# Optimization experiments

Hardware: AMD Instinct MI355X
Metric: run time of the kernel (lower is better)

Reference implementation:

```python
import jax, jax.numpy as jnp
import numpy as np

B, S = 64, 1024
D_INPUT, D_POLAR, N_LAYERS, KAN, N_CLASSES = 256, 256, 8, 32, 1000
PI = float(np.pi)
EPS = 1e-8


def _gelu(v):
    return jax.nn.gelu(v, approximate=False)  # torch nn.GELU default = exact erf


def setup_inputs() -> dict:
    key = jax.random.key(0)
    ks = jax.random.split(key, 16)

    def rn(k, shape, fan_in):
        return jax.random.normal(k, shape, jnp.float32) / np.sqrt(fan_in)

    return {
        "x": jax.random.normal(ks[0], (B, S, D_INPUT), jnp.float32),
        "embed_w": rn(ks[1], (D_INPUT, 2 * D_POLAR), D_INPUT),
        "embed_b": jnp.zeros((2 * D_POLAR,), jnp.float32),
        "mag_w1": rn(ks[2], (N_LAYERS, 1, KAN), 1),
        "mag_b1": jnp.zeros((N_LAYERS, KAN), jnp.float32),
        "mag_w2": rn(ks[3], (N_LAYERS, KAN, 1), KAN),
        "mag_b2": jnp.zeros((N_LAYERS, 1), jnp.float32),
        "ph_w1": rn(ks[4], (N_LAYERS, 2, KAN), 2),
        "ph_b1": jnp.zeros((N_LAYERS, KAN), jnp.float32),
        "ph_w2": rn(ks[5], (N_LAYERS, KAN, 2), KAN),
        "ph_b2": jnp.zeros((N_LAYERS, 2), jnp.float32),
        "cls_w1": rn(ks[6], (D_POLAR, KAN), D_POLAR),
        "cls_b1": jnp.zeros((KAN,), jnp.float32),
        "cls_w2": rn(ks[7], (KAN, N_CLASSES), KAN),
        "cls_b2": jnp.zeros((N_CLASSES,), jnp.float32),
    }


def _forward(x, embed_w, embed_b, mag_w1, mag_b1, mag_w2, mag_b2,
             ph_w1, ph_b1, ph_w2, ph_b2, cls_w1, cls_b1, cls_w2, cls_b2):
    h = x @ embed_w + embed_b                      # [B,S,2D]
    r = jnp.abs(h[..., :D_POLAR]) + 0.1            # [B,S,D]
    theta = h[..., D_POLAR:] * PI                  # [B,S,D]
    for i in range(N_LAYERS):
        xc = r * jnp.cos(theta)
        yc = r * jnp.sin(theta)
        xm = xc.mean(axis=1, keepdims=True)        # [B,1,D]
        ym = yc.mean(axis=1, keepdims=True)
        r_agg = jnp.sqrt(xm * xm + ym * ym + EPS)
        th_agg = jnp.arctan2(ym, xm)
        # magnitude MLP (1 -> 32 -> 1) in log space, per channel
        log_r = jnp.log(r_agg + EPS)[..., None]    # [B,1,D,1]
        lr = _gelu(log_r @ mag_w1[i] + mag_b1[i]) @ mag_w2[i] + mag_b2[i]
        r_trans = jnp.exp(lr[..., 0])              # [B,1,D]
        # phase MLP (2 -> 32 -> 2) on (sin, cos)
        pin = jnp.stack([jnp.sin(th_agg), jnp.cos(th_agg)], axis=-1)  # [B,1,D,2]
        pout = _gelu(pin @ ph_w1[i] + ph_b1[i]) @ ph_w2[i] + ph_b2[i]
        norm = jnp.sqrt(pout[..., 0] ** 2 + pout[..., 1] ** 2 + EPS)
        th_trans = jnp.arctan2(pout[..., 0] / norm, pout[..., 1] / norm)
        x_out = xc + r_trans * jnp.cos(th_trans)
        y_out = yc + r_trans * jnp.sin(th_trans)
        r = jnp.sqrt(x_out * x_out + y_out * y_out + EPS)
        theta = jnp.arctan2(y_out, x_out)
    pooled = r.mean(axis=1)                        # [B,D]
    return _gelu(pooled @ cls_w1 + cls_b1) @ cls_w2 + cls_b2  # [B,n_classes]


def reference(x, embed_w, embed_b, mag_w1, mag_b1, mag_w2, mag_b2,
              ph_w1, ph_b1, ph_w2, ph_b2, cls_w1, cls_b1, cls_w2, cls_b2):
    return _forward(x, embed_w, embed_b, mag_w1, mag_b1, mag_w2, mag_b2,
                    ph_w1, ph_b1, ph_w2, ph_b2, cls_w1, cls_b1, cls_w2, cls_b2)
```

## Files before the change

kernel.cpp:

```cpp
#include <hip/hip_runtime.h>
#include <hip/hip_bf16.h>
#include <hip/hip_fp16.h>

#define EPS 1e-8f
#define PI_F 3.14159265358979323846f

typedef _Float16 half8 __attribute__((ext_vector_type(8)));
typedef _Float16 half4 __attribute__((ext_vector_type(4)));
typedef float f32x4 __attribute__((ext_vector_type(4)));
typedef float f32x2 __attribute__((ext_vector_type(2)));

__device__ __forceinline__ float gelu_exact(float v) {
    return 0.5f * v * (1.0f + erff(v * 0.70710678118654752f));
}

__global__ void convertW(const float* __restrict__ W,
                         _Float16* __restrict__ Wth, _Float16* __restrict__ Wtl,
                         float* __restrict__ zero_base) {
    int idx = blockIdx.x * 256 + threadIdx.x;
    if (idx < 49152) zero_base[idx] = 0.f;
    int col = idx & 511, k = idx >> 9;
    int d = col & 255, g = d >> 6;
    int j = g * 128 + ((col < 256) ? (d & 63) : (64 + (d & 63)));
    float f = W[k * 512 + col];
    _Float16 h = (_Float16)f;
    Wth[j * 256 + k] = h;
    Wtl[j * 256 + k] = (_Float16)(f - (float)h);
}

__global__ __launch_bounds__(256, 4) void gemm_embed(
    const float* __restrict__ x,
    const _Float16* __restrict__ Wth, const _Float16* __restrict__ Wtl,
    const float* __restrict__ bias,
    unsigned short* __restrict__ XY8,
    float* __restrict__ XMsum, float* __restrict__ YMsum)
{
    __shared__ __attribute__((aligned(16))) _Float16 Ah[4096], Al[4096], Bh[4096], Bl[4096];
    const int tid  = threadIdx.x;
    const int wave = tid >> 6;
    const int lane = tid & 63;
    const int id   = blockIdx.x;
    const int xcd  = id & 7;
    const int s    = id >> 3;
    const int g    = s & 3;
    const int mt   = (s >> 2) * 8 + xcd;
    const int m0   = mt * 128;
    const int q    = lane >> 4, ln = lane & 15;

    f32x4 acc[8][2];
#pragma unroll
    for (int mi = 0; mi < 8; ++mi) {
        acc[mi][0] = (f32x4){0.f, 0.f, 0.f, 0.f};
        acc[mi][1] = (f32x4){0.f, 0.f, 0.f, 0.f};
    }

    for (int kt = 0; kt < 8; ++kt) {
        __syncthreads();
#pragma unroll
        for (int c2 = 0; c2 < 2; ++c2) {
            int idx = c2 * 256 + tid;
            int r = idx >> 2, c = idx & 3;
            size_t go = (size_t)(g * 128 + r) * 256 + kt * 32 + c * 8;
            half8 vh = *(const half8*)(Wth + go);
            half8 vl = *(const half8*)(Wtl + go);
            int pos = c ^ ((r >> 1) & 3);
            *(half8*)&Bh[r * 32 + pos * 8] = vh;
            *(half8*)&Bl[r * 32 + pos * 8] = vl;
        }
#pragma unroll
        for (int L = 0; L < 2; ++L) {
            int idx = L * 256 + tid;
            int r = idx >> 2, cq = idx & 3;
            const float* src = x + (size_t)(m0 + r) * 256 + kt * 32 + cq * 8;
            const float4 f0 = *(const float4*)(src);
            const float4 f1 = *(const float4*)(src + 4);
            half8 hh, ll;
            hh[0] = (_Float16)f0.x; ll[0] = (_Float16)(f0.x - (float)hh[0]);
            hh[1] = (_Float16)f0.y; ll[1] = (_Float16)(f0.y - (float)hh[1]);
            hh[2] = (_Float16)f0.z; ll[2] = (_Float16)(f0.z - (float)hh[2]);
            hh[3] = (_Float16)f0.w; ll[3] = (_Float16)(f0.w - (float)hh[3]);
            hh[4] = (_Float16)f1.x; ll[4] = (_Float16)(f1.x - (float)hh[4]);
            hh[5] = (_Float16)f1.y; ll[5] = (_Float16)(f1.y - (float)hh[5]);
            hh[6] = (_Float16)f1.z; ll[6] = (_Float16)(f1.z - (float)hh[6]);
            hh[7] = (_Float16)f1.w; ll[7] = (_Float16)(f1.w - (float)hh[7]);
            int pos = cq ^ ((r >> 1) & 3);
            *(half8*)&Ah[r * 32 + pos * 8] = hh;
            *(half8*)&Al[r * 32 + pos * 8] = ll;
        }
        __syncthreads();

        half8 bh[2], bl[2], am[8];
#pragma unroll
        for (int t = 0; t < 2; ++t) {
            int rn = (t * 4 + wave) * 16 + ln;
            int off = rn * 32 + (q ^ ((rn >> 1) & 3)) * 8;
            bh[t] = *(const half8*)&Bh[off];
            bl[t] = *(const half8*)&Bl[off];
        }
#pragma unroll
        for (int mi = 0; mi < 8; ++mi) {
            int row = mi * 16 + ln;
            am[mi] = *(const half8*)&Ah[row * 32 + (q ^ ((row >> 1) & 3)) * 8];
        }
#pragma unroll
        for (int mi = 0; mi < 8; ++mi)
#pragma unroll
            for (int t = 0; t < 2; ++t)
                acc[mi][t] = __builtin_amdgcn_mfma_f32_16x16x32_f16(am[mi], bh[t], acc[mi][t], 0, 0, 0);
#pragma unroll
        for (int mi = 0; mi < 8; ++mi)
#pragma unroll
            for (int t = 0; t < 2; ++t)
                acc[mi][t] = __builtin_amdgcn_mfma_f32_16x16x32_f16(am[mi], bl[t], acc[mi][t], 0, 0, 0);
#pragma unroll
        for (int mi = 0; mi < 8; ++mi) {
            int row = mi * 16 + ln;
            half8 alv = *(const half8*)&Al[row * 32 + (q ^ ((row >> 1) & 3)) * 8];
#pragma unroll
            for (int t = 0; t < 2; ++t)
                acc[mi][t] = __builtin_amdgcn_mfma_f32_16x16x32_f16(alv, bh[t], acc[mi][t], 0, 0, 0);
        }
    }

    const int d  = g * 64 + wave * 16 + ln;
    const int b  = m0 >> 10;
    const float b1 = bias[d];
    const float b2 = bias[256 + d];
    float sx = 0.f, sy = 0.f;
#pragma unroll
    for (int mi = 0; mi < 8; ++mi) {
#pragma unroll
        for (int i = 0; i < 4; ++i) {
            const int row = m0 + mi * 16 + q * 4 + i;
            const float h1 = acc[mi][0][i] + b1;
            const float h2 = acc[mi][1][i] + b2;
            const float rr = fabsf(h1) + 0.1f;
            float sv, cv;
            __sincosf(PI_F * h2, &sv, &cv);
            const float xc = rr * cv, yc = rr * sv;
            int pk = __builtin_amdgcn_cvt_pk_fp8_f32(xc, yc, 0, false);
            XY8[(size_t)row * 256 + d] = (unsigned short)pk;
            sx += xc; sy += yc;
        }
    }
    sx += __shfl_down(sx, 32); sx += __shfl_down(sx, 16);
    sy += __shfl_down(sy, 32); sy += __shfl_down(sy, 16);
    if (lane < 16) {
        atomicAdd(&XMsum[b * 256 + d], sx);
        atomicAdd(&YMsum[b * 256 + d], sy);
    }
}

__global__ __launch_bounds__(256) void layers_kernel(
    const float* __restrict__ XMsum, const float* __restrict__ YMsum,
    const float* __restrict__ mw1, const float* __restrict__ mb1,
    const float* __restrict__ mw2, const float* __restrict__ mb2,
    const float* __restrict__ pw1, const float* __restrict__ pb1,
    const float* __restrict__ pw2, const float* __restrict__ pb2,
    float* __restrict__ DX, float* __restrict__ DY)
{
    __shared__ float s_mw1[256], s_mb1[256], s_mw2[256], s_mb2[8];
    __shared__ float s_pw1[512], s_pb1[256], s_pw2[512], s_pb2[16];
    const int tid = threadIdx.x;
    s_mw1[tid] = mw1[tid]; s_mb1[tid] = mb1[tid];
    s_mw2[tid] = mw2[tid]; s_pb1[tid] = pb1[tid];
    s_pw1[tid] = pw1[tid]; s_pw1[256 + tid] = pw1[256 + tid];
    s_pw2[tid] = pw2[tid]; s_pw2[256 + tid] = pw2[256 + tid];
    if (tid < 8)  s_mb2[tid] = mb2[tid];
    if (tid < 16) s_pb2[tid] = pb2[tid];
    __syncthreads();

    const int gid = blockIdx.x * 256 + tid;
    const int idx = gid >> 3;
    const int sub = gid & 7;
    float xm = XMsum[idx] * (1.0f / 1024.0f);
    float ym = YMsum[idx] * (1.0f / 1024.0f);
    float dxa = 0.f, dya = 0.f;
#pragma unroll 1
    for (int i = 0; i < 8; ++i) {
        float r2    = xm * xm + ym * ym;
        float r_agg = sqrtf(r2 + EPS);
        float hyp   = sqrtf(r2);
        float inv   = hyp > 0.f ? 1.0f / hyp : 0.f;
        float st    = ym * inv;
        float ct    = hyp > 0.f ? xm * inv : 1.0f;
        float log_r = logf(r_agg + EPS);
        float lr = 0.f, p0 = 0.f, p1 = 0.f;
#pragma unroll
        for (int k4 = 0; k4 < 4; ++k4) {
            int k = sub * 4 + k4;
            float hm = gelu_exact(log_r * s_mw1[i * 32 + k] + s_mb1[i * 32 + k]);
            lr += hm * s_mw2[i * 32 + k];
            float hp = gelu_exact(st * s_pw1[i * 64 + k] + ct * s_pw1[i * 64 + 32 + k] + s_pb1[i * 32 + k]);
            p0 += hp * s_pw2[i * 64 + 2 * k + 0];
            p1 += hp * s_pw2[i * 64 + 2 * k + 1];
        }
        lr += __shfl_xor(lr, 1); lr += __shfl_xor(lr, 2); lr += __shfl_xor(lr, 4);
        p0 += __shfl_xor(p0, 1); p0 += __shfl_xor(p0, 2); p0 += __shfl_xor(p0, 4);
        p1 += __shfl_xor(p1, 1); p1 += __shfl_xor(p1, 2); p1 += __shfl_xor(p1, 4);
        lr += s_mb2[i];
        p0 += s_pb2[i * 2 + 0];
        p1 += s_pb2[i * 2 + 1];
        float r_trans = expf(lr);
        float hp2  = sqrtf(p0 * p0 + p1 * p1);
        float invp = hp2 > 0.f ? 1.0f / hp2 : 0.f;
        float ctt  = hp2 > 0.f ? p1 * invp : 1.0f;
        float stt  = p0 * invp;
        float dx = r_trans * ctt;
        float dy = r_trans * stt;
        dxa += dx; dya += dy; xm += dx; ym += dy;
    }
    if (sub == 0) { DX[idx] = dxa; DY[idx] = dya; }
}

__global__ __launch_bounds__(256) void pool_kernel(
    const unsigned short* __restrict__ XY8,
    const float* __restrict__ DX, const float* __restrict__ DY,
    float* __restrict__ pooled)
{
    __shared__ float red[256][9];
    const int b = blockIdx.x, sc = blockIdx.y, tid = threadIdx.x;
    const int dg = tid & 31;
    const int sh = tid >> 5;
    const int d0 = dg * 8;
    float dxv[8], dyv[8], s[8];
#pragma unroll
    for (int j = 0; j < 8; ++j) {
        dxv[j] = DX[b * 256 + d0 + j];
        dyv[j] = DY[b * 256 + d0 + j];
        s[j] = 0.f;
    }
    const int r0 = sc * 128 + sh * 16;
    const size_t base = ((size_t)b * 1024 + r0) * 256 + d0;
#pragma unroll 4
    for (int i = 0; i < 16; ++i) {
        const int4 v = *(const int4*)(XY8 + base + (size_t)i * 256);
        const int wv[4] = {v.x, v.y, v.z, v.w};
#pragma unroll
        for (int w = 0; w < 4; ++w) {
            f32x2 pa = __builtin_amdgcn_cvt_pk_f32_fp8(wv[w], false);
            f32x2 pb = __builtin_amdgcn_cvt_pk_f32_fp8(wv[w], true);
            float xa = pa[0] + dxv[2 * w],     ya = pa[1] + dyv[2 * w];
            float xb = pb[0] + dxv[2 * w + 1], yb = pb[1] + dyv[2 * w + 1];
            s[2 * w]     += sqrtf(xa * xa + ya * ya + EPS);
            s[2 * w + 1] += sqrtf(xb * xb + yb * yb + EPS);
        }
    }
#pragma unroll
    for (int j = 0; j < 8; ++j) red[tid][j] = s[j];
    __syncthreads();
    if (tid < 32) {
#pragma unroll
        for (int j = 0; j < 8; ++j) {
            float t = 0.f;
#pragma unroll
            for (int c = 0; c < 8; ++c) t += red[c * 32 + tid][j];
            atomicAdd(&pooled[b * 256 + tid * 8 + j], t);
        }
    }
}

__global__ __launch_bounds__(256) void cls_kernel(
    const float* __restrict__ pooled,
    const float* __restrict__ w1, const float* __restrict__ b1,
    const float* __restrict__ w2, const float* __restrict__ b2,
    float* __restrict__ out)
{
    __shared__ float pl[256];
    __shared__ float part[8][32];
    __shared__ float hd[32];
    const int b = blockIdx.x, tid = threadIdx.x;
    pl[tid] = pooled[b * 256 + tid] * (1.0f / 1024.0f);
    __syncthreads();
    const int hu = tid & 31, kc = tid >> 5;
    float a = 0.f;
    for (int k = kc * 32; k < kc * 32 + 32; ++k) a += pl[k] * w1[k * 32 + hu];
    part[kc][hu] = a;
    __syncthreads();
    if (tid < 32) {
        float s = b1[tid];
#pragma unroll
        for (int c = 0; c < 8; ++c) s += part[c][tid];
        hd[tid] = gelu_exact(s);
    }
    __syncthreads();
    for (int n = tid; n < 1000; n += 256) {
        float s = b2[n];
#pragma unroll
        for (int k = 0; k < 32; ++k) s += hd[k] * w2[k * 1000 + n];
        out[b * 1000 + n] = s;
    }
}

extern "C" void kernel_launch(void* const* d_in, const int* in_sizes, int n_in,
                              void* d_out, int out_size, void* d_ws, size_t ws_size,
                              hipStream_t stream)
{
    const float* x       = (const float*)d_in[0];
    const float* embed_w = (const float*)d_in[1];
    const float* embed_b = (const float*)d_in[2];
    const float* mag_w1  = (const float*)d_in[3];
    const float* mag_b1  = (const float*)d_in[4];
    const float* mag_w2  = (const float*)d_in[5];
    const float* mag_b2  = (const float*)d_in[6];
    const float* ph_w1   = (const float*)d_in[7];
    const float* ph_b1   = (const float*)d_in[8];
    const float* ph_w2   = (const float*)d_in[9];
    const float* ph_b2   = (const float*)d_in[10];
    const float* cls_w1  = (const float*)d_in[11];
    const float* cls_b1  = (const float*)d_in[12];
    const float* cls_w2  = (const float*)d_in[13];
    const float* cls_b2  = (const float*)d_in[14];
    float* out = (float*)d_out;

    char* ws = (char*)d_ws;
    unsigned short* XY8 = (unsigned short*)(ws + 0);
    _Float16* Wth = (_Float16*)(ws + 33554432);
    _Float16* Wtl = (_Float16*)(ws + 33816576);
    float* XMsum  = (float*)(ws + 34078720);
    float* YMsum  = (float*)(ws + 34144256);
    float* pooled = (float*)(ws + 34209792);
    float* DX     = (float*)(ws + 34275328);
    float* DY     = (float*)(ws + 34340864);

    convertW<<<512, 256, 0, stream>>>(embed_w, Wth, Wtl, XMsum);
    gemm_embed<<<2048, 256, 0, stream>>>(x, Wth, Wtl, embed_b, XY8, XMsum, YMsum);
    layers_kernel<<<512, 256, 0, stream>>>(XMsum, YMsum, mag_w1, mag_b1, mag_w2, mag_b2,
                                           ph_w1, ph_b1, ph_w2, ph_b2, DX, DY);
    pool_kernel<<<dim3(64, 8), 256, 0, stream>>>(XY8, DX, DY, pooled);
    cls_kernel<<<64, 256, 0, stream>>>(pooled, cls_w1, cls_b1, cls_w2, cls_b2, out);
}
```

Before: 211.2 us.

## Load embed GEMM B fragments directly from pre-tiled global weights; split classifier

```diff
diff --git a/kernel.cpp b/kernel.cpp
--- a/kernel.cpp
+++ b/kernel.cpp
@@ -20,12 +20,16 @@
     int idx = blockIdx.x * 256 + threadIdx.x;
     if (idx < 49152) zero_base[idx] = 0.f;
     int col = idx & 511, k = idx >> 9;
-    int d = col & 255, g = d >> 6;
-    int j = g * 128 + ((col < 256) ? (d & 63) : (64 + (d & 63)));
+    int d  = col & 255;
+    int g  = d >> 6;
+    int dl = d & 63;
+    int r  = (dl >> 5) * 64 + ((col >> 8) << 5) + (dl & 31);
+    int kt = k >> 5, ko = k & 31;
     float f = W[k * 512 + col];
     _Float16 h = (_Float16)f;
-    Wth[j * 256 + k] = h;
-    Wtl[j * 256 + k] = (_Float16)(f - (float)h);
+    int o = ((g * 8 + kt) * 128 + r) * 32 + ko;
+    Wth[o] = h;
+    Wtl[o] = (_Float16)(f - (float)h);
 }
 
 __global__ __launch_bounds__(256, 4) void gemm_embed(
@@ -35,10 +39,12 @@
     unsigned short* __restrict__ XY8,
     float* __restrict__ XMsum, float* __restrict__ YMsum)
 {
-    __shared__ __attribute__((aligned(16))) _Float16 Ah[4096], Al[4096], Bh[4096], Bl[4096];
+    __shared__ __attribute__((aligned(16))) _Float16 Ah[4096], Al[4096];
     const int tid  = threadIdx.x;
     const int wave = tid >> 6;
     const int lane = tid & 63;
+    const int wm   = wave >> 1;
+    const int wn   = wave & 1;
     const int id   = blockIdx.x;
     const int xcd  = id & 7;
     const int s    = id >> 3;
@@ -47,30 +53,29 @@
     const int m0   = mt * 128;
     const int q    = lane >> 4, ln = lane & 15;
 
-    f32x4 acc[8][2];
-#pragma unroll
-    for (int mi = 0; mi < 8; ++mi) {
-        acc[mi][0] = (f32x4){0.f, 0.f, 0.f, 0.f};
-        acc[mi][1] = (f32x4){0.f, 0.f, 0.f, 0.f};
-    }
+    f32x4 acc[4][4];
+#pragma unroll
+    for (int mi = 0; mi < 4; ++mi)
+#pragma unroll
+        for (int nt = 0; nt < 4; ++nt)
+            acc[mi][nt] = (f32x4){0.f, 0.f, 0.f, 0.f};
 
     for (int kt = 0; kt < 8; ++kt) {
+        half8 bh[4], bl[4];
+        {
+            const int tbase = (g * 8 + kt) * 4096;
+#pragma unroll
+            for (int nt = 0; nt < 4; ++nt) {
+                int off = tbase + (wn * 64 + nt * 16 + ln) * 32 + q * 8;
+                bh[nt] = *(const half8*)(Wth + off);
+                bl[nt] = *(const half8*)(Wtl + off);
+            }
+        }
         __syncthreads();
 #pragma unroll
-        for (int c2 = 0; c2 < 2; ++c2) {
-            int idx = c2 * 256 + tid;
-            int r = idx >> 2, c = idx & 3;
-            size_t go = (size_t)(g * 128 + r) * 256 + kt * 32 + c * 8;
-            half8 vh = *(const half8*)(Wth + go);
-            half8 vl = *(const half8*)(Wtl + go);
-            int pos = c ^ ((r >> 1) & 3);
-            *(half8*)&Bh[r * 32 + pos * 8] = vh;
-            *(half8*)&Bl[r * 32 + pos * 8] = vl;
-        }
-#pragma unroll
         for (int L = 0; L < 2; ++L) {
-            int idx = L * 256 + tid;
-            int r = idx >> 2, cq = idx & 3;
+            int idx2 = L * 256 + tid;
+            int r = idx2 >> 2, cq = idx2 & 3;
             const float* src = x + (size_t)(m0 + r) * 256 + kt * 32 + cq * 8;
             const float4 f0 = *(const float4*)(src);
             const float4 f1 = *(const float4*)(src + 4);
@@ -89,65 +94,76 @@
         }
         __syncthreads();
 
-        half8 bh[2], bl[2], am[8];
-#pragma unroll
-        for (int t = 0; t < 2; ++t) {
-            int rn = (t * 4 + wave) * 16 + ln;
-            int off = rn * 32 + (q ^ ((rn >> 1) & 3)) * 8;
-            bh[t] = *(const half8*)&Bh[off];
-            bl[t] = *(const half8*)&Bl[off];
-        }
-#pragma unroll
-        for (int mi = 0; mi < 8; ++mi) {
-            int row = mi * 16 + ln;
+        half8 am[4];
+#pragma unroll
+        for (int mi = 0; mi < 4; ++mi) {
+            int row = wm * 64 + mi * 16 + ln;
             am[mi] = *(const half8*)&Ah[row * 32 + (q ^ ((row >> 1) & 3)) * 8];
         }
 #pragma unroll
-        for (int mi = 0; mi < 8; ++mi)
-#pragma unroll
-            for (int t = 0; t < 2; ++t)
-                acc[mi][t] = __builtin_amdgcn_mfma_f32_16x16x32_f16(am[mi], bh[t], acc[mi][t], 0, 0, 0);
-#pragma unroll
-        for (int mi = 0; mi < 8; ++mi)
-#pragma unroll
-            for (int t = 0; t < 2; ++t)
-                acc[mi][t] = __builtin_amdgcn_mfma_f32_16x16x32_f16(am[mi], bl[t], acc[mi][t], 0, 0, 0);
-#pragma unroll
-        for (int mi = 0; mi < 8; ++mi) {
-            int row = mi * 16 + ln;
+        for (int mi = 0; mi < 4; ++mi)
+#pragma unroll
+            for (int nt = 0; nt < 4; ++nt)
+                acc[mi][nt] = __builtin_amdgcn_mfma_f32_16x16x32_f16(am[mi], bh[nt], acc[mi][nt], 0, 0, 0);
+#pragma unroll
+        for (int mi = 0; mi < 4; ++mi)
+#pragma unroll
+            for (int nt = 0; nt < 4; ++nt)
+                acc[mi][nt] = __builtin_amdgcn_mfma_f32_16x16x32_f16(am[mi], bl[nt], acc[mi][nt], 0, 0, 0);
+#pragma unroll
+        for (int mi = 0; mi < 4; ++mi) {
+            int row = wm * 64 + mi * 16 + ln;
             half8 alv = *(const half8*)&Al[row * 32 + (q ^ ((row >> 1) & 3)) * 8];
 #pragma unroll
-            for (int t = 0; t < 2; ++t)
-                acc[mi][t] = __builtin_amdgcn_mfma_f32_16x16x32_f16(alv, bh[t], acc[mi][t], 0, 0, 0);
-        }
-    }
-
-    const int d  = g * 64 + wave * 16 + ln;
+            for (int nt = 0; nt < 4; ++nt)
+                acc[mi][nt] = __builtin_amdgcn_mfma_f32_16x16x32_f16(alv, bh[nt], acc[mi][nt], 0, 0, 0);
+        }
+    }
+
+    const int d0 = g * 64 + wn * 32 + ln;
+    const int d1 = d0 + 16;
     const int b  = m0 >> 10;
-    const float b1 = bias[d];
-    const float b2 = bias[256 + d];
-    float sx = 0.f, sy = 0.f;
-#pragma unroll
-    for (int mi = 0; mi < 8; ++mi) {
+    const float b1_0 = bias[d0],       b1_1 = bias[d1];
+    const float b2_0 = bias[256 + d0], b2_1 = bias[256 + d1];
+    float sx0 = 0.f, sy0 = 0.f, sx1 = 0.f, sy1 = 0.f;
+#pragma unroll
+    for (int mi = 0; mi < 4; ++mi) {
 #pragma unroll
         for (int i = 0; i < 4; ++i) {
-            const int row = m0 + mi * 16 + q * 4 + i;
-            const float h1 = acc[mi][0][i] + b1;
-            const float h2 = acc[mi][1][i] + b2;
-            const float rr = fabsf(h1) + 0.1f;
-            float sv, cv;
-            __sincosf(PI_F * h2, &sv, &cv);
-            const float xc = rr * cv, yc = rr * sv;
-            int pk = __builtin_amdgcn_cvt_pk_fp8_f32(xc, yc, 0, false);
-            XY8[(size_t)row * 256 + d] = (unsigned short)pk;
-            sx += xc; sy += yc;
-        }
-    }
-    sx += __shfl_down(sx, 32); sx += __shfl_down(sx, 16);
-    sy += __shfl_down(sy, 32); sy += __shfl_down(sy, 16);
+            const int row = m0 + wm * 64 + mi * 16 + q * 4 + i;
+            {
+                const float h1 = acc[mi][0][i] + b1_0;
+                const float h2 = acc[mi][2][i] + b2_0;
+                const float rr = fabsf(h1) + 0.1f;
+                float sv, cv;
+                __sincosf(PI_F * h2, &sv, &cv);
+                const float xc = rr * cv, yc = rr * sv;
+                int pk = __builtin_amdgcn_cvt_pk_fp8_f32(xc, yc, 0, false);
+                XY8[(size_t)row * 256 + d0] = (unsigned short)pk;
+                sx0 += xc; sy0 += yc;
+            }
+            {
+                const float h1 = acc[mi][1][i] + b1_1;
+                const float h2 = acc[mi][3][i] + b2_1;
+                const float rr = fabsf(h1) + 0.1f;
+                float sv, cv;
+                __sincosf(PI_F * h2, &sv, &cv);
+                const float xc = rr * cv, yc = rr * sv;
+                int pk = __builtin_amdgcn_cvt_pk_fp8_f32(xc, yc, 0, false);
+                XY8[(size_t)row * 256 + d1] = (unsigned short)pk;
+                sx1 += xc; sy1 += yc;
+            }
+        }
+    }
+    sx0 += __shfl_down(sx0, 32); sx0 += __shfl_down(sx0, 16);
+    sy0 += __shfl_down(sy0, 32); sy0 += __shfl_down(sy0, 16);
+    sx1 += __shfl_down(sx1, 32); sx1 += __shfl_down(sx1, 16);
+    sy1 += __shfl_down(sy1, 32); sy1 += __shfl_down(sy1, 16);
     if (lane < 16) {
-        atomicAdd(&XMsum[b * 256 + d], sx);
-        atomicAdd(&YMsum[b * 256 + d], sy);
+        atomicAdd(&XMsum[b * 256 + d0], sx0);
+        atomicAdd(&YMsum[b * 256 + d0], sy0);
+        atomicAdd(&XMsum[b * 256 + d1], sx1);
+        atomicAdd(&YMsum[b * 256 + d1], sy1);
     }
 }
 
@@ -269,7 +285,7 @@
     __shared__ float pl[256];
     __shared__ float part[8][32];
     __shared__ float hd[32];
-    const int b = blockIdx.x, tid = threadIdx.x;
+    const int b = blockIdx.x, yc = blockIdx.y, tid = threadIdx.x;
     pl[tid] = pooled[b * 256 + tid] * (1.0f / 1024.0f);
     __syncthreads();
     const int hu = tid & 31, kc = tid >> 5;
@@ -284,7 +300,9 @@
         hd[tid] = gelu_exact(s);
     }
     __syncthreads();
-    for (int n = tid; n < 1000; n += 256) {
+    const int n0 = yc * 250;
+    const int nend = (n0 + 250 < 1000) ? n0 + 250 : 1000;
+    for (int n = n0 + tid; n < nend; n += 256) {
         float s = b2[n];
 #pragma unroll
         for (int k = 0; k < 32; ++k) s += hd[k] * w2[k * 1000 + n];
@@ -328,5 +346,5 @@
     layers_kernel<<<512, 256, 0, stream>>>(XMsum, YMsum, mag_w1, mag_b1, mag_w2, mag_b2,
                                            ph_w1, ph_b1, ph_w2, ph_b2, DX, DY);
     pool_kernel<<<dim3(64, 8), 256, 0, stream>>>(XY8, DX, DY, pooled);
-    cls_kernel<<<64, 256, 0, stream>>>(pooled, cls_w1, cls_b1, cls_w2, cls_b2, out);
-}
+    cls_kernel<<<dim3(64, 4), 256, 0, stream>>>(pooled, cls_w1, cls_b1, cls_w2, cls_b2, out);
+}
```

After: 204.2 us. 1.03x faster.
